# Kernel tuning notes

Measured on AMD Instinct MI355X. Metric: run time of the kernel, lower is better.

Reference implementation:

```python
import jax, jax.numpy as jnp
import numpy as np

T, B, E, H = 2048, 4, 1024, 16
D = E // H  # head_dim = 64


def setup_inputs() -> dict:
    key = jax.random.key(0)
    k0, k1, k2 = jax.random.split(key, 3)
    std = (2.0 / (E + E)) ** 0.5  # matches reset_parameters
    inp = jax.random.normal(k0, (T, B, E), jnp.float32)
    in_w = jax.random.normal(k1, (3 * E, E), jnp.float32) * std
    in_b = jnp.zeros((3 * E,), jnp.float32)
    out_w = jax.random.normal(k2, (E, E), jnp.float32) * std
    out_b = jnp.zeros((E,), jnp.float32)
    # standard RoPE angle table, duplicated across halves so rotate_half pairing is exact
    inv_freq = 1.0 / (10000.0 ** (jnp.arange(0, D, 2, dtype=jnp.float32) / D))  # [D/2]
    ang = jnp.arange(T, dtype=jnp.float32)[:, None] * inv_freq[None, :]          # [T, D/2]
    pos = jnp.concatenate([ang, ang], axis=-1)                                    # [T, D]
    attn_mask = jnp.triu(jnp.ones((T, T), dtype=bool), k=1)  # True = masked (future)
    return {
        "input": inp,
        "pos": pos,
        "in_proj_weight": in_w,
        "in_proj_bias": in_b,
        "out_proj_weight": out_w,
        "out_proj_bias": out_b,
        "attn_mask": attn_mask,
    }


def _rotate_half(x):
    x1, x2 = jnp.split(x, 2, axis=-1)
    return jnp.concatenate([-x2, x1], axis=-1)


def reference(input, pos, in_proj_weight, in_proj_bias, out_proj_weight,
              out_proj_bias, attn_mask):
    Tq, Bq, Eq = input.shape
    nh = H
    hd = Eq // nh
    scaling = hd ** -0.5
    # fused QKV projection: [T,B,3E]
    qkv = input @ in_proj_weight.T + in_proj_bias
    q, k, v = jnp.split(qkv, 3, axis=-1)
    q = q.reshape(Tq, Bq, nh, hd)
    k = k.reshape(Tq, Bq, nh, hd)
    v = v.reshape(Tq, Bq, nh, hd)
    # rotary positional encoding applied inline to q and k
    cos = jnp.cos(pos)[:, None, None, :]  # [T,1,1,D]
    sin = jnp.sin(pos)[:, None, None, :]
    q = q * cos + _rotate_half(q) * sin
    k = k * cos + _rotate_half(k) * sin
    q = q * scaling
    # attention scores [B,H,T,S]
    scores = jnp.einsum('tbhd,sbhd->bhts', q, k)
    scores = jnp.where(attn_mask[None, None, :, :], -jnp.inf, scores)
    attn = jax.nn.softmax(scores, axis=-1)  # coverage
    ctx = jnp.einsum('bhts,sbhd->tbhd', attn, v).reshape(Tq, Bq, Eq)
    out = ctx @ out_proj_weight.T + out_proj_bias
    return out, attn
```

## Files before the change

### kernel.cpp

```cpp
#include <hip/hip_runtime.h>

typedef unsigned short u16;
typedef unsigned int u32;

#define TT 2048
#define BB 4
#define EE 1024
#define HH 16
#define DD 64
#define LOG2E 1.4426950408889634f

typedef __bf16 bf16x8 __attribute__((ext_vector_type(8)));
typedef float f32x4 __attribute__((ext_vector_type(4)));

__device__ __forceinline__ f32x4 mfma16(bf16x8 a, bf16x8 b, f32x4 c) {
  return __builtin_amdgcn_mfma_f32_16x16x32_bf16(a, b, c, 0, 0, 0);
}

__device__ __forceinline__ u16 f2bf(float f) {
  u32 u = __float_as_uint(f);
  u += 0x7fffu + ((u >> 16) & 1u);
  return (u16)(u >> 16);
}
__device__ __forceinline__ float bf2f(u16 u) {
  return __uint_as_float(((u32)u) << 16);
}

__device__ __forceinline__ void load_lds16(const void* g, void* l) {
  __builtin_amdgcn_global_load_lds((const __attribute__((address_space(1))) u32*)g,
                                   (__attribute__((address_space(3))) u32*)l, 16, 0, 0);
}

__global__ __launch_bounds__(256) void cvt_kernel(const float* __restrict__ in,
                                                  u16* __restrict__ out, int n4) {
  int i = blockIdx.x * 256 + threadIdx.x;
  if (i >= n4) return;
  float4 v = ((const float4*)in)[i];
  u32 lo = (u32)f2bf(v.x) | ((u32)f2bf(v.y) << 16);
  u32 hi = (u32)f2bf(v.z) | ((u32)f2bf(v.w) << 16);
  ((uint2*)out)[i] = make_uint2(lo, hi);
}

template<bool BF16_OUT>
__global__ __launch_bounds__(256) void gemm_bt(const u16* __restrict__ A,
    const u16* __restrict__ B, const float* __restrict__ bias,
    void* __restrict__ Cp, int M, int N, int K)
{
  __shared__ u16 As[128 * 32];
  __shared__ u16 Bs[128 * 32];
  const int tid = threadIdx.x;
  const int m0 = blockIdx.y * 128;
  const int n0 = blockIdx.x * 128;
  const int w = tid >> 6, lane = tid & 63;
  const int quad = lane >> 4, l16 = lane & 15;
  const int wm = (w & 1) * 64, wn = (w >> 1) * 64;

  const f32x4 zero4 = {0.f, 0.f, 0.f, 0.f};
  f32x4 acc[4][4];
#pragma unroll
  for (int i = 0; i < 4; i++)
#pragma unroll
    for (int j = 0; j < 4; j++) acc[i][j] = zero4;

  for (int k0 = 0; k0 < K; k0 += 32) {
#pragma unroll
    for (int i = 0; i < 2; i++) {
      int c = i * 256 + tid;
      int row = c >> 2, col = (c & 3) * 8;
      load_lds16(A + (size_t)(m0 + row) * K + k0 + col, &As[c * 8]);
      load_lds16(B + (size_t)(n0 + row) * K + k0 + col, &Bs[c * 8]);
    }
    __syncthreads();
    bf16x8 af[4], bfr[4];
#pragma unroll
    for (int i = 0; i < 4; i++)
      af[i] = *(const bf16x8*)&As[(wm + i * 16 + l16) * 32 + quad * 8];
#pragma unroll
    for (int j = 0; j < 4; j++)
      bfr[j] = *(const bf16x8*)&Bs[(wn + j * 16 + l16) * 32 + quad * 8];
#pragma unroll
    for (int i = 0; i < 4; i++)
#pragma unroll
      for (int j = 0; j < 4; j++)
        acc[i][j] = mfma16(af[i], bfr[j], acc[i][j]);
    __syncthreads();
  }
#pragma unroll
  for (int i = 0; i < 4; i++)
#pragma unroll
    for (int j = 0; j < 4; j++) {
      int col = n0 + wn + j * 16 + l16;
      float bv = bias[col];
#pragma unroll
      for (int r = 0; r < 4; r++) {
        int row = m0 + wm + i * 16 + quad * 4 + r;
        float v = acc[i][j][r] + bv;
        if (BF16_OUT) ((u16*)Cp)[(size_t)row * N + col] = f2bf(v);
        else          ((float*)Cp)[(size_t)row * N + col] = v;
      }
    }
}

__global__ __launch_bounds__(256) void rope_kernel(const u16* __restrict__ qkv,
    const float* __restrict__ pos, u16* __restrict__ Qg, u16* __restrict__ Kg)
{
  int u = blockIdx.x * 256 + threadIdx.x;
  int d0 = (u & 15) * 4;
  int h = (u >> 4) & 15;
  int m = u >> 8;
  int t = m >> 2, b = m & 3;
  const u16* rowq = qkv + (size_t)m * 3072 + h * 64;
  uint2 qa = *(const uint2*)(rowq + d0);
  uint2 qb = *(const uint2*)(rowq + (d0 ^ 32));
  uint2 ka = *(const uint2*)(rowq + 1024 + d0);
  uint2 kb = *(const uint2*)(rowq + 1024 + (d0 ^ 32));
  float qv[4] = {bf2f((u16)(qa.x & 0xffff)), bf2f((u16)(qa.x >> 16)),
                 bf2f((u16)(qa.y & 0xffff)), bf2f((u16)(qa.y >> 16))};
  float qp[4] = {bf2f((u16)(qb.x & 0xffff)), bf2f((u16)(qb.x >> 16)),
                 bf2f((u16)(qb.y & 0xffff)), bf2f((u16)(qb.y >> 16))};
  float kv[4] = {bf2f((u16)(ka.x & 0xffff)), bf2f((u16)(ka.x >> 16)),
                 bf2f((u16)(ka.y & 0xffff)), bf2f((u16)(ka.y >> 16))};
  float kp[4] = {bf2f((u16)(kb.x & 0xffff)), bf2f((u16)(kb.x >> 16)),
                 bf2f((u16)(kb.y & 0xffff)), bf2f((u16)(kb.y >> 16))};
  float sgn = (d0 < 32) ? -1.f : 1.f;
  float qo[4], ko[4];
#pragma unroll
  for (int i = 0; i < 4; i++) {
    float a = pos[t * 64 + d0 + i];
    float sv, cv;
    sincosf(a, &sv, &cv);
    qo[i] = (qv[i] * cv + sgn * qp[i] * sv) * 0.125f;
    ko[i] = kv[i] * cv + sgn * kp[i] * sv;
  }
  size_t obase = ((size_t)(b * 16 + h) * TT + t) * 64 + d0;
  *(uint2*)(Qg + obase) = make_uint2((u32)f2bf(qo[0]) | ((u32)f2bf(qo[1]) << 16),
                                     (u32)f2bf(qo[2]) | ((u32)f2bf(qo[3]) << 16));
  *(uint2*)(Kg + obase) = make_uint2((u32)f2bf(ko[0]) | ((u32)f2bf(ko[1]) << 16),
                                     (u32)f2bf(ko[2]) | ((u32)f2bf(ko[3]) << 16));
}

__global__ __launch_bounds__(256) void vtrans_kernel(const u16* __restrict__ qkv,
                                                     u16* __restrict__ Vt)
{
  __shared__ u16 Ls[64 * 64];
  int bh = blockIdx.y, b = bh >> 4, h = bh & 15;
  int t0 = blockIdx.x * 64;
  int tid = threadIdx.x;
#pragma unroll
  for (int i = 0; i < 2; i++) {
    int c = i * 256 + tid;
    int r = c >> 3, ch = c & 7;
    int m = (t0 + r) * 4 + b;
    uint4 v = *(const uint4*)(qkv + (size_t)m * 3072 + 2048 + h * 64 + ch * 8);
    *(uint4*)&Ls[r * 64 + ((ch ^ (r & 7)) * 8)] = v;
  }
  __syncthreads();
#pragma unroll
  for (int i = 0; i < 2; i++) {
    int u = i * 256 + tid;
    int d = u >> 3, tc = u & 7;
    u32 pk[4];
#pragma unroll
    for (int p = 0; p < 4; p++) {
      int r0 = tc * 8 + p * 2, r1 = r0 + 1;
      u16 a = Ls[r0 * 64 + (((d >> 3) ^ (r0 & 7)) * 8) + (d & 7)];
      u16 bb = Ls[r1 * 64 + (((d >> 3) ^ (r1 & 7)) * 8) + (d & 7)];
      pk[p] = (u32)a | ((u32)bb << 16);
    }
    *(uint4*)(Vt + ((size_t)bh * 64 + d) * TT + t0 + tc * 8) =
        make_uint4(pk[0], pk[1], pk[2], pk[3]);
  }
}

__global__ __launch_bounds__(256) void attn_kernel(const u16* __restrict__ Qg,
    const u16* __restrict__ Kg, const u16* __restrict__ Vt,
    float* __restrict__ attn, u16* __restrict__ ctx)
{
  __shared__ u16 Ks[128 * 64];
  __shared__ u16 Vs[64 * 128];
  __shared__ u16 QPs[128 * 64];

  const int bh = blockIdx.y;
  const int qt = (int)gridDim.x - 1 - (int)blockIdx.x;
  const int b = bh >> 4, h = bh & 15;
  const int q0 = qt * 128;
  const int tid = threadIdx.x;
  const int w = tid >> 6, lane = tid & 63;
  const int quad = lane >> 4, l16 = lane & 15;
  const f32x4 zero4 = {0.f, 0.f, 0.f, 0.f};

  {
    const u16* src = Qg + ((size_t)bh * TT + q0) * 64;
#pragma unroll
    for (int i = 0; i < 4; i++) {
      int c = i * 256 + tid;
      int row = c >> 3, ch = c & 7;
      uint4 v = *(const uint4*)(src + row * 64 + ch * 8);
      *(uint4*)&QPs[row * 64 + ((ch ^ (row & 7)) * 8)] = v;
    }
  }
  __syncthreads();
  bf16x8 aq[2][2];
#pragma unroll
  for (int i = 0; i < 2; i++)
#pragma unroll
    for (int ks = 0; ks < 2; ks++) {
      int row = w * 32 + i * 16 + l16;
      int ch = (ks * 4 + quad) ^ (row & 7);
      aq[i][ks] = *(const bf16x8*)&QPs[row * 64 + ch * 8];
    }
  __syncthreads();

  float mrow[8], lrow[8];
#pragma unroll
  for (int x = 0; x < 8; x++) { mrow[x] = -1e30f; lrow[x] = 0.f; }

  for (int kt = 0; kt <= qt; kt++) {
    const u16* src = Kg + ((size_t)bh * TT + kt * 128) * 64;
#pragma unroll
    for (int i = 0; i < 4; i++) {
      int c = i * 256 + tid;
      int row = c >> 3, ch = c & 7;
      uint4 v = *(const uint4*)(src + row * 64 + ch * 8);
      *(uint4*)&Ks[row * 64 + ((ch ^ (row & 7)) * 8)] = v;
    }
    __syncthreads();
    f32x4 sacc[2][8];
#pragma unroll
    for (int i = 0; i < 2; i++)
#pragma unroll
      for (int j = 0; j < 8; j++) sacc[i][j] = zero4;
#pragma unroll
    for (int ks = 0; ks < 2; ks++)
#pragma unroll
      for (int j = 0; j < 8; j++) {
        int row = j * 16 + l16;
        int ch = (ks * 4 + quad) ^ (row & 7);
        bf16x8 bk = *(const bf16x8*)&Ks[row * 64 + ch * 8];
        sacc[0][j] = mfma16(aq[0][ks], bk, sacc[0][j]);
        sacc[1][j] = mfma16(aq[1][ks], bk, sacc[1][j]);
      }
    if (kt == qt) {
#pragma unroll
      for (int i = 0; i < 2; i++)
#pragma unroll
        for (int j = 0; j < 8; j++) {
          int scol = j * 16 + l16;
#pragma unroll
          for (int r = 0; r < 4; r++) {
            int trow = w * 32 + i * 16 + quad * 4 + r;
            if (scol > trow) sacc[i][j][r] = -1e30f;
          }
        }
    }
#pragma unroll
    for (int i = 0; i < 2; i++)
#pragma unroll
      for (int r = 0; r < 4; r++) {
        float mx = sacc[i][0][r];
#pragma unroll
        for (int j = 1; j < 8; j++) mx = fmaxf(mx, sacc[i][j][r]);
#pragma unroll
        for (int off = 1; off < 16; off <<= 1) mx = fmaxf(mx, __shfl_xor(mx, off));
        int idx = i * 4 + r;
        float mnew = fmaxf(mrow[idx], mx);
        float s = 0.f;
#pragma unroll
        for (int j = 0; j < 8; j++) s += exp2f((sacc[i][j][r] - mnew) * LOG2E);
#pragma unroll
        for (int off = 1; off < 16; off <<= 1) s += __shfl_xor(s, off);
        lrow[idx] = lrow[idx] * exp2f((mrow[idx] - mnew) * LOG2E) + s;
        mrow[idx] = mnew;
      }
    __syncthreads();
  }

  float inv_l[8];
#pragma unroll
  for (int x = 0; x < 8; x++) inv_l[x] = 1.f / lrow[x];

  f32x4 cacc[2][4];
#pragma unroll
  for (int i = 0; i < 2; i++)
#pragma unroll
    for (int j = 0; j < 4; j++) cacc[i][j] = zero4;

  for (int kt = 0; kt <= qt; kt++) {
    int s0 = kt * 128;
    const u16* srcK = Kg + ((size_t)bh * TT + s0) * 64;
    const u16* srcV = Vt + (size_t)bh * 64 * TT + s0;
#pragma unroll
    for (int i = 0; i < 4; i++) {
      int c = i * 256 + tid;
      { int row = c >> 3, ch = c & 7;
        uint4 v = *(const uint4*)(srcK + row * 64 + ch * 8);
        *(uint4*)&Ks[row * 64 + ((ch ^ (row & 7)) * 8)] = v; }
      { int d = c >> 4, ch = c & 15;
        uint4 v = *(const uint4*)(srcV + (size_t)d * TT + ch * 8);
        *(uint4*)&Vs[d * 128 + ((ch ^ (d & 15)) * 8)] = v; }
    }
    __syncthreads();
    f32x4 sacc[2][8];
#pragma unroll
    for (int i = 0; i < 2; i++)
#pragma unroll
      for (int j = 0; j < 8; j++) sacc[i][j] = zero4;
#pragma unroll
    for (int ks = 0; ks < 2; ks++)
#pragma unroll
      for (int j = 0; j < 8; j++) {
        int row = j * 16 + l16;
        int ch = (ks * 4 + quad) ^ (row & 7);
        bf16x8 bk = *(const bf16x8*)&Ks[row * 64 + ch * 8];
        sacc[0][j] = mfma16(aq[0][ks], bk, sacc[0][j]);
        sacc[1][j] = mfma16(aq[1][ks], bk, sacc[1][j]);
      }
    if (kt == qt) {
#pragma unroll
      for (int i = 0; i < 2; i++)
#pragma unroll
        for (int j = 0; j < 8; j++) {
          int scol = j * 16 + l16;
#pragma unroll
          for (int r = 0; r < 4; r++) {
            int trow = w * 32 + i * 16 + quad * 4 + r;
            if (scol > trow) sacc[i][j][r] = -1e30f;
          }
        }
    }
    float* abase = attn + ((size_t)bh * TT + q0) * TT + s0;
#pragma unroll
    for (int hf = 0; hf < 2; hf++) {
#pragma unroll
      for (int i = 0; i < 2; i++)
#pragma unroll
        for (int jl = 0; jl < 4; jl++) {
          int j = hf * 4 + jl;
#pragma unroll
          for (int r = 0; r < 4; r++) {
            int tr = w * 32 + i * 16 + quad * 4 + r;
            float p = exp2f((sacc[i][j][r] - mrow[i * 4 + r]) * LOG2E) * inv_l[i * 4 + r];
            abase[(size_t)tr * TT + j * 16 + l16] = p;
            int sc = jl * 16 + l16;
            QPs[tr * 64 + (((sc >> 3) ^ (tr & 7)) * 8) + (sc & 7)] = f2bf(p);
          }
        }
#pragma unroll
      for (int ks2 = 0; ks2 < 2; ks2++) {
        bf16x8 ap[2];
#pragma unroll
        for (int i = 0; i < 2; i++) {
          int row = w * 32 + i * 16 + l16;
          int ch = (ks2 * 4 + quad) ^ (row & 7);
          ap[i] = *(const bf16x8*)&QPs[row * 64 + ch * 8];
        }
#pragma unroll
        for (int j = 0; j < 4; j++) {
          int drow = j * 16 + l16;
          int ch = (hf * 8 + ks2 * 4 + quad) ^ (drow & 15);
          bf16x8 bv = *(const bf16x8*)&Vs[drow * 128 + ch * 8];
          cacc[0][j] = mfma16(ap[0], bv, cacc[0][j]);
          cacc[1][j] = mfma16(ap[1], bv, cacc[1][j]);
        }
      }
    }
    __syncthreads();
  }

#pragma unroll
  for (int i = 0; i < 2; i++)
#pragma unroll
    for (int j = 0; j < 4; j++)
#pragma unroll
      for (int r = 0; r < 4; r++) {
        int tr = q0 + w * 32 + i * 16 + quad * 4 + r;
        int d = j * 16 + l16;
        ctx[((size_t)tr * BB + b) * EE + h * 64 + d] = f2bf(cacc[i][j][r]);
      }

  int nz4 = (15 - qt) * 32;
  if (nz4 > 0) {
    float4 z = make_float4(0.f, 0.f, 0.f, 0.f);
    float* base = attn + ((size_t)bh * TT + q0) * TT + (qt + 1) * 128;
    for (int r = 0; r < 128; r++)
      for (int c4 = tid; c4 < nz4; c4 += 256)
        *(float4*)(base + (size_t)r * TT + c4 * 4) = z;
  }
}

extern "C" void kernel_launch(void* const* d_in, const int* in_sizes, int n_in,
                              void* d_out, int out_size, void* d_ws, size_t ws_size,
                              hipStream_t stream) {
  (void)in_sizes; (void)n_in; (void)out_size; (void)ws_size;
  const float* input = (const float*)d_in[0];
  const float* pos   = (const float*)d_in[1];
  const float* in_w  = (const float*)d_in[2];
  const float* in_b  = (const float*)d_in[3];
  const float* out_w = (const float*)d_in[4];
  const float* out_b = (const float*)d_in[5];

  float* out  = (float*)d_out;
  float* attn = out + (size_t)TT * BB * EE;

  char* ws = (char*)d_ws;
  u16* inA = (u16*)ws;
  u16* w1b = (u16*)(ws + 16777216);
  u16* w2b = (u16*)(ws + 23068672);
  u16* Qg  = (u16*)(ws + 25165824);
  u16* Kg  = (u16*)(ws + 41943040);
  u16* Vt  = (u16*)(ws + 58720256);
  u16* ctx = inA;
  u16* qkv = (u16*)attn;

  cvt_kernel<<<8192, 256, 0, stream>>>(input, inA, 2097152);
  cvt_kernel<<<3072, 256, 0, stream>>>(in_w, w1b, 786432);
  cvt_kernel<<<1024, 256, 0, stream>>>(out_w, w2b, 262144);
  gemm_bt<true><<<dim3(24, 64), 256, 0, stream>>>(inA, w1b, in_b, (void*)qkv,
                                                  8192, 3072, 1024);
  rope_kernel<<<8192, 256, 0, stream>>>(qkv, pos, Qg, Kg);
  vtrans_kernel<<<dim3(32, 64), 256, 0, stream>>>(qkv, Vt);
  attn_kernel<<<dim3(16, 64), 256, 0, stream>>>(Qg, Kg, Vt, attn, ctx);
  gemm_bt<false><<<dim3(8, 64), 256, 0, stream>>>(ctx, w2b, out_b, (void*)out,
                                                  8192, 1024, 1024);
}
```

Baseline: 1.695 ms.

## Double-buffer K/V tiles via direct LDS loads and defer softmax lane reductions

Double-buffers the K and V shared-memory tiles and issues the next tile's loads through load_lds16 direct global-to-LDS copies before computing on the current tile, so loads overlap MFMA work. The per-tile cross-lane max/sum shuffles in the statistics pass are replaced by per-lane online softmax state, merged once after the loop. The log2(e) factor is folded into the Q scaling so exp2f needs no multiply, and launch bounds request two blocks per CU. In exchange LDS use per block roughly doubles, and correctness depends on load_lds16 waiting for its copies before each barrier.

```diff
diff --git a/kernel.cpp b/kernel.cpp
--- a/kernel.cpp
+++ b/kernel.cpp
@@ -129,7 +129,7 @@
     float a = pos[t * 64 + d0 + i];
     float sv, cv;
     sincosf(a, &sv, &cv);
-    qo[i] = (qv[i] * cv + sgn * qp[i] * sv) * 0.125f;
+    qo[i] = (qv[i] * cv + sgn * qp[i] * sv) * 0.18033688f;
     ko[i] = kv[i] * cv + sgn * kp[i] * sv;
   }
   size_t obase = ((size_t)(b * 16 + h) * TT + t) * 64 + d0;
@@ -172,12 +172,12 @@
   }
 }
 
-__global__ __launch_bounds__(256) void attn_kernel(const u16* __restrict__ Qg,
+__global__ __launch_bounds__(256, 2) void attn_kernel(const u16* __restrict__ Qg,
     const u16* __restrict__ Kg, const u16* __restrict__ Vt,
     float* __restrict__ attn, u16* __restrict__ ctx)
 {
-  __shared__ u16 Ks[128 * 64];
-  __shared__ u16 Vs[64 * 128];
+  __shared__ u16 Ks[2][128 * 64];
+  __shared__ u16 Vs[2][64 * 128];
   __shared__ u16 QPs[128 * 64];
 
   const int bh = blockIdx.y;
@@ -189,17 +189,40 @@
   const int quad = lane >> 4, l16 = lane & 15;
   const f32x4 zero4 = {0.f, 0.f, 0.f, 0.f};
 
+  const u16* Kbase = Kg + (size_t)bh * TT * 64;
+  const u16* Vbase = Vt + (size_t)bh * 64 * TT;
+
+  auto stageK = [&](int buf, int kt) {
+    const u16* src = Kbase + (size_t)kt * 128 * 64;
+#pragma unroll
+    for (int i = 0; i < 4; i++) {
+      int c = i * 256 + tid;
+      int row = c >> 3, chl = c & 7;
+      load_lds16(src + row * 64 + ((chl ^ (row & 7)) * 8), &Ks[buf][c * 8]);
+    }
+  };
+  auto stageV = [&](int buf, int kt) {
+    const u16* src = Vbase + kt * 128;
+#pragma unroll
+    for (int i = 0; i < 4; i++) {
+      int c = i * 256 + tid;
+      int d = c >> 4, chl = c & 15;
+      load_lds16(src + (size_t)d * TT + ((chl ^ (d & 15)) * 8), &Vs[buf][c * 8]);
+    }
+  };
+
   {
     const u16* src = Qg + ((size_t)bh * TT + q0) * 64;
 #pragma unroll
     for (int i = 0; i < 4; i++) {
       int c = i * 256 + tid;
-      int row = c >> 3, ch = c & 7;
-      uint4 v = *(const uint4*)(src + row * 64 + ch * 8);
-      *(uint4*)&QPs[row * 64 + ((ch ^ (row & 7)) * 8)] = v;
-    }
-  }
+      int row = c >> 3, chl = c & 7;
+      load_lds16(src + row * 64 + ((chl ^ (row & 7)) * 8), &QPs[c * 8]);
+    }
+  }
+  stageK(0, 0);
   __syncthreads();
+
   bf16x8 aq[2][2];
 #pragma unroll
   for (int i = 0; i < 2; i++)
@@ -215,16 +238,9 @@
 #pragma unroll
   for (int x = 0; x < 8; x++) { mrow[x] = -1e30f; lrow[x] = 0.f; }
 
+  int cur = 0;
   for (int kt = 0; kt <= qt; kt++) {
-    const u16* src = Kg + ((size_t)bh * TT + kt * 128) * 64;
-#pragma unroll
-    for (int i = 0; i < 4; i++) {
-      int c = i * 256 + tid;
-      int row = c >> 3, ch = c & 7;
-      uint4 v = *(const uint4*)(src + row * 64 + ch * 8);
-      *(uint4*)&Ks[row * 64 + ((ch ^ (row & 7)) * 8)] = v;
-    }
-    __syncthreads();
+    if (kt < qt) stageK(cur ^ 1, kt + 1);
     f32x4 sacc[2][8];
 #pragma unroll
     for (int i = 0; i < 2; i++)
@@ -236,7 +252,7 @@
       for (int j = 0; j < 8; j++) {
         int row = j * 16 + l16;
         int ch = (ks * 4 + quad) ^ (row & 7);
-        bf16x8 bk = *(const bf16x8*)&Ks[row * 64 + ch * 8];
+        bf16x8 bk = *(const bf16x8*)&Ks[cur][row * 64 + ch * 8];
         sacc[0][j] = mfma16(aq[0][ks], bk, sacc[0][j]);
         sacc[1][j] = mfma16(aq[1][ks], bk, sacc[1][j]);
       }
@@ -257,27 +273,38 @@
     for (int i = 0; i < 2; i++)
 #pragma unroll
       for (int r = 0; r < 4; r++) {
-        float mx = sacc[i][0][r];
-#pragma unroll
-        for (int j = 1; j < 8; j++) mx = fmaxf(mx, sacc[i][j][r]);
-#pragma unroll
-        for (int off = 1; off < 16; off <<= 1) mx = fmaxf(mx, __shfl_xor(mx, off));
         int idx = i * 4 + r;
+        float a0 = fmaxf(sacc[i][0][r], sacc[i][1][r]);
+        float a1 = fmaxf(sacc[i][2][r], sacc[i][3][r]);
+        float a2 = fmaxf(sacc[i][4][r], sacc[i][5][r]);
+        float a3 = fmaxf(sacc[i][6][r], sacc[i][7][r]);
+        float mx = fmaxf(fmaxf(a0, a1), fmaxf(a2, a3));
         float mnew = fmaxf(mrow[idx], mx);
         float s = 0.f;
 #pragma unroll
-        for (int j = 0; j < 8; j++) s += exp2f((sacc[i][j][r] - mnew) * LOG2E);
-#pragma unroll
-        for (int off = 1; off < 16; off <<= 1) s += __shfl_xor(s, off);
-        lrow[idx] = lrow[idx] * exp2f((mrow[idx] - mnew) * LOG2E) + s;
+        for (int j = 0; j < 8; j++) s += exp2f(sacc[i][j][r] - mnew);
+        lrow[idx] = lrow[idx] * exp2f(mrow[idx] - mnew) + s;
         mrow[idx] = mnew;
       }
     __syncthreads();
+    cur ^= 1;
   }
 
   float inv_l[8];
 #pragma unroll
-  for (int x = 0; x < 8; x++) inv_l[x] = 1.f / lrow[x];
+  for (int idx = 0; idx < 8; idx++) {
+    float m = mrow[idx], l = lrow[idx];
+#pragma unroll
+    for (int off = 1; off < 16; off <<= 1) {
+      float mo = __shfl_xor(m, off);
+      float lo = __shfl_xor(l, off);
+      float mn = fmaxf(m, mo);
+      l = l * exp2f(m - mn) + lo * exp2f(mo - mn);
+      m = mn;
+    }
+    mrow[idx] = m;
+    inv_l[idx] = 1.f / l;
+  }
 
   f32x4 cacc[2][4];
 #pragma unroll
@@ -285,21 +312,11 @@
 #pragma unroll
     for (int j = 0; j < 4; j++) cacc[i][j] = zero4;
 
+  stageK(cur, 0);
+  stageV(cur, 0);
+  __syncthreads();
   for (int kt = 0; kt <= qt; kt++) {
-    int s0 = kt * 128;
-    const u16* srcK = Kg + ((size_t)bh * TT + s0) * 64;
-    const u16* srcV = Vt + (size_t)bh * 64 * TT + s0;
-#pragma unroll
-    for (int i = 0; i < 4; i++) {
-      int c = i * 256 + tid;
-      { int row = c >> 3, ch = c & 7;
-        uint4 v = *(const uint4*)(srcK + row * 64 + ch * 8);
-        *(uint4*)&Ks[row * 64 + ((ch ^ (row & 7)) * 8)] = v; }
-      { int d = c >> 4, ch = c & 15;
-        uint4 v = *(const uint4*)(srcV + (size_t)d * TT + ch * 8);
-        *(uint4*)&Vs[d * 128 + ((ch ^ (d & 15)) * 8)] = v; }
-    }
-    __syncthreads();
+    if (kt < qt) { stageK(cur ^ 1, kt + 1); stageV(cur ^ 1, kt + 1); }
     f32x4 sacc[2][8];
 #pragma unroll
     for (int i = 0; i < 2; i++)
@@ -311,7 +328,7 @@
       for (int j = 0; j < 8; j++) {
         int row = j * 16 + l16;
         int ch = (ks * 4 + quad) ^ (row & 7);
-        bf16x8 bk = *(const bf16x8*)&Ks[row * 64 + ch * 8];
+        bf16x8 bk = *(const bf16x8*)&Ks[cur][row * 64 + ch * 8];
         sacc[0][j] = mfma16(aq[0][ks], bk, sacc[0][j]);
         sacc[1][j] = mfma16(aq[1][ks], bk, sacc[1][j]);
       }
@@ -328,7 +345,7 @@
           }
         }
     }
-    float* abase = attn + ((size_t)bh * TT + q0) * TT + s0;
+    float* abase = attn + ((size_t)bh * TT + q0) * TT + kt * 128;
 #pragma unroll
     for (int hf = 0; hf < 2; hf++) {
 #pragma unroll
@@ -339,7 +356,7 @@
 #pragma unroll
           for (int r = 0; r < 4; r++) {
             int tr = w * 32 + i * 16 + quad * 4 + r;
-            float p = exp2f((sacc[i][j][r] - mrow[i * 4 + r]) * LOG2E) * inv_l[i * 4 + r];
+            float p = exp2f(sacc[i][j][r] - mrow[i * 4 + r]) * inv_l[i * 4 + r];
             abase[(size_t)tr * TT + j * 16 + l16] = p;
             int sc = jl * 16 + l16;
             QPs[tr * 64 + (((sc >> 3) ^ (tr & 7)) * 8) + (sc & 7)] = f2bf(p);
@@ -358,13 +375,14 @@
         for (int j = 0; j < 4; j++) {
           int drow = j * 16 + l16;
           int ch = (hf * 8 + ks2 * 4 + quad) ^ (drow & 15);
-          bf16x8 bv = *(const bf16x8*)&Vs[drow * 128 + ch * 8];
+          bf16x8 bv = *(const bf16x8*)&Vs[cur][drow * 128 + ch * 8];
           cacc[0][j] = mfma16(ap[0], bv, cacc[0][j]);
           cacc[1][j] = mfma16(ap[1], bv, cacc[1][j]);
         }
       }
     }
     __syncthreads();
+    cur ^= 1;
   }
 
 #pragma unroll
```

Result: slower. 1.892 ms (+11.6%).
